# Kernel tuning notes

Measured on AMD Instinct MI355X. Metric: run time of the kernel, lower is better.

The kernel has to match this reference:

```python
import jax, jax.numpy as jnp
import numpy as np

DN = ('NCDHW', 'OIDHW', 'NCDHW')

def conv3d(x, w, b):
    # kernel (1,3,3), stride 1, padding (0,1,1)
    y = jax.lax.conv_general_dilated(x, w, window_strides=(1, 1, 1),
                                     padding=[(0, 0), (1, 1), (1, 1)],
                                     dimension_numbers=DN)
    return y + b[None, :, None, None, None]

def setup_inputs() -> dict:
    key = jax.random.key(0)
    ks = jax.random.split(key, 9)
    B, C, S, H, W = 16, 64, 64, 32, 32
    Cd = C // 2
    fan = C * 9
    sc = 1.0 / np.sqrt(fan)
    x = jax.random.normal(ks[0], (B, C, S, H, W), jnp.float32)
    wq = jax.random.normal(ks[1], (Cd, C, 1, 3, 3), jnp.float32) * sc
    bq = jax.random.normal(ks[2], (Cd,), jnp.float32) * sc
    wk = jax.random.normal(ks[3], (Cd, C, 1, 3, 3), jnp.float32) * sc
    bk = jax.random.normal(ks[4], (Cd,), jnp.float32) * sc
    wv = jax.random.normal(ks[5], (Cd, C, 1, 3, 3), jnp.float32) * sc
    bv = jax.random.normal(ks[6], (Cd,), jnp.float32) * sc
    wo = jax.random.normal(ks[7], (C, Cd, 1, 3, 3), jnp.float32) * (1.0 / np.sqrt(Cd * 9))
    bo = jax.random.normal(ks[8], (C,), jnp.float32) * (1.0 / np.sqrt(Cd * 9))
    return {"x": x, "wq": wq, "bq": bq, "wk": wk, "bk": bk,
            "wv": wv, "bv": bv, "wo": wo, "bo": bo}

def reference(x, wq, bq, wk, bk, wv, bv, wo, bo):
    B, C, S, H, W = x.shape
    scale = (H * W) ** (-0.5)
    q = conv3d(x, wq, bq).reshape(B, -1, S, H * W)  # (B, Cd, S, HW)
    k = conv3d(x, wk, bk).reshape(B, -1, S, H * W)
    v = conv3d(x, wv, bv).reshape(B, -1, S, H * W)
    # per-channel attention over sequence dim with sigmoid gate
    attn = jax.nn.sigmoid(jnp.einsum('bcsf,bctf->bcst', q, k) * scale)  # (B, Cd, S, S)
    out = jnp.einsum('bcst,bctf->bcsf', attn, v)  # (B, Cd, S, HW)
    out = out.reshape(B, -1, S, H, W)
    return conv3d(out, wo, bo)
```

## Files before the change

kernel.cpp:

```cpp
#include <hip/hip_runtime.h>
#include <hip/hip_bf16.h>

#define BB   16
#define CC   64
#define SS   64
#define HWHW 1024
#define CD   32
#define QELEMS (BB * CD * SS * HWHW)

typedef unsigned short ushort_t;
typedef __attribute__((ext_vector_type(8)))  short bf16x8;
typedef __attribute__((ext_vector_type(16))) float f32x16;

static __device__ inline float bf2f(ushort_t u) {
    union { float f; unsigned int i; } v;
    v.i = ((unsigned int)u) << 16;
    return v.f;
}
static __device__ inline ushort_t f2bf(float f) {
    union { float f; unsigned int i; } v;
    v.f = f;
    unsigned int x = v.i;
    return (ushort_t)((x + 0x7fffu + ((x >> 16) & 1u)) >> 16);
}

__global__ __launch_bounds__(256) void pack_weights(
    const float* __restrict__ wq, const float* __restrict__ wk,
    const float* __restrict__ wv, const float* __restrict__ wo,
    ushort_t* __restrict__ wt, ushort_t* __restrict__ wt2)
{
    const int d = blockIdx.x * 256 + threadIdx.x;
    if (d < 9 * 96 * 64) {
        const int tap = d / (96 * 64);
        const int rem = d % (96 * 64);
        const int oc  = rem >> 6;
        const int c   = rem & 63;
        const float* wsrc = (oc < 32) ? wq : (oc < 64) ? wk : wv;
        const int ocl = oc & 31;
        wt[d] = f2bf(wsrc[((size_t)ocl * 64 + c) * 9 + tap]);
    }
    const int d2 = d - 9 * 96 * 64;
    if (d2 >= 0 && d2 < 9 * 64 * 32) {
        const int tap = d2 / (64 * 32);
        const int rem = d2 % (64 * 32);
        const int oc  = rem >> 5;
        const int c   = rem & 31;
        wt2[d2] = f2bf(wo[((size_t)oc * 32 + c) * 9 + tap]);
    }
}

__global__ __launch_bounds__(256) void conv_qkv_mfma(
    const float* __restrict__ x,
    const ushort_t* __restrict__ wt,
    const float* __restrict__ bq, const float* __restrict__ bk,
    const float* __restrict__ bv,
    ushort_t* __restrict__ qkv)
{
    __shared__ ushort_t xs[10][34][72];

    const int tid   = threadIdx.x;
    const int bs    = blockIdx.x >> 2;
    const int chunk = blockIdx.x & 3;
    const int b     = bs >> 6;
    const int s     = bs & 63;
    const int h0    = chunk * 8;

    if (tid < 160) {
        const int r    = tid >> 4;
        const int rest = tid & 15;
        const int col  = (rest >> 3) ? 33 : 0;
        const int c0   = (rest & 7) << 3;
        bf16x8 z = {0, 0, 0, 0, 0, 0, 0, 0};
        *(bf16x8*)&xs[r][col][c0] = z;
    }

    const float* xb = x + ((size_t)b * CC * SS + s) * HWHW;
#pragma unroll
    for (int it = 0; it < 20; ++it) {
        const int u  = tid + it * 256;
        const int g  = u & 7;
        const int t2 = u >> 3;
        const int r  = t2 % 10;
        const int c  = t2 / 10;
        const int h  = h0 - 1 + r;
        float4 xv = make_float4(0.f, 0.f, 0.f, 0.f);
        if (h >= 0 && h < 32)
            xv = *(const float4*)(xb + (size_t)c * SS * HWHW + h * 32 + g * 4);
        const int colb = 1 + g * 4;
        xs[r][colb + 0][c] = f2bf(xv.x);
        xs[r][colb + 1][c] = f2bf(xv.y);
        xs[r][colb + 2][c] = f2bf(xv.z);
        xs[r][colb + 3][c] = f2bf(xv.w);
    }
    __syncthreads();

    const int wvid = tid >> 6;
    const int lane = tid & 63;
    const int ln   = lane & 31;
    const int lh   = lane >> 5;
    const int nt0  = wvid * 2;

    f32x16 acc[3][2];
#pragma unroll
    for (int m = 0; m < 3; ++m)
#pragma unroll
        for (int n = 0; n < 2; ++n)
#pragma unroll
            for (int i = 0; i < 16; ++i) acc[m][n][i] = 0.f;

#pragma unroll 1
    for (int tap = 0; tap < 9; ++tap) {
        const int dh = tap / 3;
        const int dw = tap % 3;
        const ushort_t* wtap = wt + (size_t)tap * 96 * 64;
#pragma unroll
        for (int kc = 0; kc < 4; ++kc) {
            const int c0 = kc * 16 + lh * 8;
            const bf16x8 a0 = *(const bf16x8*)(wtap + (((size_t)ln      ) << 6) + c0);
            const bf16x8 a1 = *(const bf16x8*)(wtap + (((size_t)ln + 32 ) << 6) + c0);
            const bf16x8 a2 = *(const bf16x8*)(wtap + (((size_t)ln + 64 ) << 6) + c0);
            const bf16x8 b0 = *(const bf16x8*)&xs[nt0 + dh    ][ln + dw][c0];
            const bf16x8 b1 = *(const bf16x8*)&xs[nt0 + 1 + dh][ln + dw][c0];
            acc[0][0] = __builtin_amdgcn_mfma_f32_32x32x16_bf16(a0, b0, acc[0][0], 0, 0, 0);
            acc[0][1] = __builtin_amdgcn_mfma_f32_32x32x16_bf16(a0, b1, acc[0][1], 0, 0, 0);
            acc[1][0] = __builtin_amdgcn_mfma_f32_32x32x16_bf16(a1, b0, acc[1][0], 0, 0, 0);
            acc[1][1] = __builtin_amdgcn_mfma_f32_32x32x16_bf16(a1, b1, acc[1][1], 0, 0, 0);
            acc[2][0] = __builtin_amdgcn_mfma_f32_32x32x16_bf16(a2, b0, acc[2][0], 0, 0, 0);
            acc[2][1] = __builtin_amdgcn_mfma_f32_32x32x16_bf16(a2, b1, acc[2][1], 0, 0, 0);
        }
    }

    const float* biases[3] = {bq, bk, bv};
#pragma unroll
    for (int mt = 0; mt < 3; ++mt) {
        const float* bptr = biases[mt];
        ushort_t* dst = qkv + (size_t)mt * QELEMS + (((size_t)b * CD) * SS + s) * HWHW;
#pragma unroll
        for (int ntl = 0; ntl < 2; ++ntl) {
            const int gp = (h0 + nt0 + ntl) * 32 + ln;
#pragma unroll
            for (int r = 0; r < 16; ++r) {
                const int m = (r & 3) + 8 * (r >> 2) + 4 * lh;
                const float val = acc[mt][ntl][r] + bptr[m];
                dst[(size_t)m * SS * HWHW + gp] = f2bf(val);
            }
        }
    }
}

__global__ __launch_bounds__(256) void attn_kernel(ushort_t* __restrict__ qkv)
{
    __shared__ float    scb[64][65];
    __shared__ ushort_t qch[64][132];
    __shared__ ushort_t kch[64][132];

    const int tid = threadIdx.x;
    const int bc  = blockIdx.x;
    ushort_t* qbase = qkv + (size_t)bc * SS * HWHW;
    const ushort_t* kbase = qbase + QELEMS;
    const ushort_t* vbase = qbase + 2 * (size_t)QELEMS;

    const int ty = tid >> 4, tx = tid & 15;
    const int sy = ty * 4, sx = tx * 4;

    float acc[4][4];
#pragma unroll
    for (int i = 0; i < 4; ++i)
#pragma unroll
        for (int j = 0; j < 4; ++j) acc[i][j] = 0.0f;

    for (int fc = 0; fc < 8; ++fc) {
        __syncthreads();
#pragma unroll
        for (int u = 0; u < 8; ++u) {
            const int unit = tid + u * 256;
            const int row  = unit >> 5;
            const int col  = (unit & 31) * 4;
            const ushort4 qa = *(const ushort4*)(qbase + (size_t)row * HWHW + fc * 128 + col);
            const ushort4 ka = *(const ushort4*)(kbase + (size_t)row * HWHW + fc * 128 + col);
            *(ushort4*)&qch[row][col] = qa;
            *(ushort4*)&kch[row][col] = ka;
        }
        __syncthreads();

        for (int f = 0; f < 128; f += 2) {
            float q0[4], q1[4], k0[4], k1[4];
#pragma unroll
            for (int i = 0; i < 4; ++i) {
                const unsigned int qp = *(const unsigned int*)&qch[sy + i][f];
                q0[i] = bf2f((ushort_t)(qp & 0xffffu));
                q1[i] = bf2f((ushort_t)(qp >> 16));
                const unsigned int kp = *(const unsigned int*)&kch[sx + i][f];
                k0[i] = bf2f((ushort_t)(kp & 0xffffu));
                k1[i] = bf2f((ushort_t)(kp >> 16));
            }
#pragma unroll
            for (int i = 0; i < 4; ++i)
#pragma unroll
                for (int j = 0; j < 4; ++j)
                    acc[i][j] += q0[i] * k0[j] + q1[i] * k1[j];
        }
    }

    const float scale = 0.03125f;
#pragma unroll
    for (int i = 0; i < 4; ++i)
#pragma unroll
        for (int j = 0; j < 4; ++j) {
            const float xv = acc[i][j] * scale;
            scb[sy + i][sx + j] = 1.0f / (1.0f + __expf(-xv));
        }
    __syncthreads();

    const int fcol = tid * 4;
#pragma unroll 1
    for (int gIdx = 0; gIdx < 4; ++gIdx) {
        float o[16][4];
#pragma unroll
        for (int i = 0; i < 16; ++i)
#pragma unroll
            for (int j = 0; j < 4; ++j) o[i][j] = 0.0f;

        for (int t = 0; t < 64; ++t) {
            const ushort4 va = *(const ushort4*)(vbase + (size_t)t * HWHW + fcol);
            const float v0 = bf2f(va.x), v1 = bf2f(va.y), v2 = bf2f(va.z), v3 = bf2f(va.w);
#pragma unroll
            for (int i = 0; i < 16; ++i) {
                const float a = scb[gIdx * 16 + i][t];
                o[i][0] += a * v0;
                o[i][1] += a * v1;
                o[i][2] += a * v2;
                o[i][3] += a * v3;
            }
        }
#pragma unroll
        for (int i = 0; i < 16; ++i) {
            const int srow = gIdx * 16 + i;
            ushort4 u;
            u.x = f2bf(o[i][0]);
            u.y = f2bf(o[i][1]);
            u.z = f2bf(o[i][2]);
            u.w = f2bf(o[i][3]);
            *(ushort4*)(qbase + (size_t)srow * HWHW + fcol) = u;
        }
    }
}

__global__ __launch_bounds__(256) void conv_out_mfma(
    const ushort_t* __restrict__ att,
    const ushort_t* __restrict__ wt2,
    const float* __restrict__ bo,
    float* __restrict__ out)
{
    __shared__ ushort_t xs[10][34][40];

    const int tid   = threadIdx.x;
    const int bs    = blockIdx.x >> 2;
    const int chunk = blockIdx.x & 3;
    const int b     = bs >> 6;
    const int s     = bs & 63;
    const int h0    = chunk * 8;

    if (tid < 80) {
        const int r    = tid >> 3;
        const int rest = tid & 7;
        const int col  = (rest >> 2) ? 33 : 0;
        const int c0   = (rest & 3) << 3;
        bf16x8 z = {0, 0, 0, 0, 0, 0, 0, 0};
        *(bf16x8*)&xs[r][col][c0] = z;
    }

    const ushort_t* ab = att + ((size_t)b * CD * SS + s) * HWHW;
#pragma unroll
    for (int it = 0; it < 10; ++it) {
        const int u  = tid + it * 256;
        const int g  = u & 7;
        const int t2 = u >> 3;
        const int r  = t2 % 10;
        const int c  = t2 / 10;
        const int h  = h0 - 1 + r;
        ushort4 xv = make_ushort4(0, 0, 0, 0);
        if (h >= 0 && h < 32)
            xv = *(const ushort4*)(ab + (size_t)c * SS * HWHW + h * 32 + g * 4);
        const int colb = 1 + g * 4;
        xs[r][colb + 0][c] = xv.x;
        xs[r][colb + 1][c] = xv.y;
        xs[r][colb + 2][c] = xv.z;
        xs[r][colb + 3][c] = xv.w;
    }
    __syncthreads();

    const int wvid = tid >> 6;
    const int lane = tid & 63;
    const int ln   = lane & 31;
    const int lh   = lane >> 5;
    const int nt0  = wvid * 2;

    f32x16 acc[2][2];
#pragma unroll
    for (int m = 0; m < 2; ++m)
#pragma unroll
        for (int n = 0; n < 2; ++n)
#pragma unroll
            for (int i = 0; i < 16; ++i) acc[m][n][i] = 0.f;

#pragma unroll 1
    for (int tap = 0; tap < 9; ++tap) {
        const int dh = tap / 3;
        const int dw = tap % 3;
        const ushort_t* wtap = wt2 + (size_t)tap * 64 * 32;
#pragma unroll
        for (int kc = 0; kc < 2; ++kc) {
            const int c0 = kc * 16 + lh * 8;
            const bf16x8 a0 = *(const bf16x8*)(wtap + (((size_t)ln      ) << 5) + c0);
            const bf16x8 a1 = *(const bf16x8*)(wtap + (((size_t)ln + 32 ) << 5) + c0);
            const bf16x8 b0 = *(const bf16x8*)&xs[nt0 + dh    ][ln + dw][c0];
            const bf16x8 b1 = *(const bf16x8*)&xs[nt0 + 1 + dh][ln + dw][c0];
            acc[0][0] = __builtin_amdgcn_mfma_f32_32x32x16_bf16(a0, b0, acc[0][0], 0, 0, 0);
            acc[0][1] = __builtin_amdgcn_mfma_f32_32x32x16_bf16(a0, b1, acc[0][1], 0, 0, 0);
            acc[1][0] = __builtin_amdgcn_mfma_f32_32x32x16_bf16(a1, b0, acc[1][0], 0, 0, 0);
            acc[1][1] = __builtin_amdgcn_mfma_f32_32x32x16_bf16(a1, b1, acc[1][1], 0, 0, 0);
        }
    }

#pragma unroll
    for (int mt = 0; mt < 2; ++mt) {
        float* dst = out + (((size_t)b * CC + mt * 32) * SS + s) * HWHW;
#pragma unroll
        for (int ntl = 0; ntl < 2; ++ntl) {
            const int gp = (h0 + nt0 + ntl) * 32 + ln;
#pragma unroll
            for (int r = 0; r < 16; ++r) {
                const int m = (r & 3) + 8 * (r >> 2) + 4 * lh;
                dst[(size_t)m * SS * HWHW + gp] = acc[mt][ntl][r] + bo[mt * 32 + m];
            }
        }
    }
}

extern "C" void kernel_launch(void* const* d_in, const int* in_sizes, int n_in,
                              void* d_out, int out_size, void* d_ws, size_t ws_size,
                              hipStream_t stream)
{
    const float* x  = (const float*)d_in[0];
    const float* wq = (const float*)d_in[1];
    const float* bq = (const float*)d_in[2];
    const float* wk = (const float*)d_in[3];
    const float* bk = (const float*)d_in[4];
    const float* wv = (const float*)d_in[5];
    const float* bv = (const float*)d_in[6];
    const float* wo = (const float*)d_in[7];
    const float* bo = (const float*)d_in[8];
    float* out = (float*)d_out;

    ushort_t* qkv = (ushort_t*)d_ws;
    ushort_t* wt  = (ushort_t*)((char*)d_ws + (size_t)3 * QELEMS * 2);
    ushort_t* wt2 = wt + 9 * 96 * 64;

    pack_weights<<<288, 256, 0, stream>>>(wq, wk, wv, wo, wt, wt2);
    conv_qkv_mfma<<<dim3(BB * SS * 4), 256, 0, stream>>>(x, wt, bq, bk, bv, qkv);
    attn_kernel<<<dim3(BB * CD), 256, 0, stream>>>(qkv);
    conv_out_mfma<<<dim3(BB * SS * 4), 256, 0, stream>>>(qkv, wt2, bo, out);
}
```

Measured before the change: 1.083 ms.

## Pre-transpose conv inputs to channel-last bf16 for vectorized tile loads

Adds two transpose kernels that convert x (fp32 NCDHW) and the attention output into per-(b,s) pixel-major, channel-contiguous bf16 buffers. Both conv kernels then fill their LDS tiles with 16-byte vector loads and stores instead of scalar strided LDS writes with a per-element conversion. The xT buffer reuses the output buffer as scratch and attT reuses the K slot of the qkv workspace. The cost is two extra launches and an extra full read and write pass over the input and attention tensors.

```diff
diff --git a/kernel.cpp b/kernel.cpp
--- a/kernel.cpp
+++ b/kernel.cpp
@@ -49,8 +49,82 @@
     }
 }
 
+__global__ __launch_bounds__(256) void transpose_x(
+    const float* __restrict__ x, ushort_t* __restrict__ xT)
+{
+    __shared__ ushort_t t[64][132];
+
+    const int bs  = blockIdx.x;
+    const int b   = bs >> 6;
+    const int s   = bs & 63;
+    const int tid = threadIdx.x;
+    const float* xb = x + ((size_t)b * CC * SS + s) * HWHW;
+    ushort_t*    xo = xT + (size_t)bs * HWHW * CC;
+
+    for (int fc = 0; fc < 8; ++fc) {
+        __syncthreads();
+#pragma unroll
+        for (int i = 0; i < 8; ++i) {
+            const int u  = tid + i * 256;
+            const int c  = u >> 5;
+            const int f4 = u & 31;
+            const float4 v = *(const float4*)(xb + (size_t)c * SS * HWHW + fc * 128 + f4 * 4);
+            const unsigned int lo = (unsigned int)f2bf(v.x) | ((unsigned int)f2bf(v.y) << 16);
+            const unsigned int hi = (unsigned int)f2bf(v.z) | ((unsigned int)f2bf(v.w) << 16);
+            *(uint2*)&t[c][f4 * 4] = make_uint2(lo, hi);
+        }
+        __syncthreads();
+#pragma unroll
+        for (int i = 0; i < 4; ++i) {
+            const int u  = tid + i * 256;
+            const int px = u >> 3;
+            const int cg = (u & 7) * 8;
+            bf16x8 vv;
+#pragma unroll
+            for (int j = 0; j < 8; ++j) vv[j] = (short)t[cg + j][px];
+            *(bf16x8*)(xo + (size_t)(fc * 128 + px) * CC + cg) = vv;
+        }
+    }
+}
+
+__global__ __launch_bounds__(256) void transpose_att(
+    const ushort_t* __restrict__ att, ushort_t* __restrict__ attT)
+{
+    __shared__ ushort_t t[32][260];
+
+    const int bs  = blockIdx.x;
+    const int b   = bs >> 6;
+    const int s   = bs & 63;
+    const int tid = threadIdx.x;
+    const ushort_t* ab = att + ((size_t)b * CD * SS + s) * HWHW;
+    ushort_t*       ao = attT + (size_t)bs * HWHW * CD;
+
+    for (int fc = 0; fc < 4; ++fc) {
+        __syncthreads();
+#pragma unroll
+        for (int i = 0; i < 8; ++i) {
+            const int u  = tid + i * 256;
+            const int c  = u >> 6;
+            const int f4 = u & 63;
+            const ushort4 v = *(const ushort4*)(ab + (size_t)c * SS * HWHW + fc * 256 + f4 * 4);
+            *(ushort4*)&t[c][f4 * 4] = v;
+        }
+        __syncthreads();
+#pragma unroll
+        for (int i = 0; i < 4; ++i) {
+            const int u  = tid + i * 256;
+            const int px = u >> 2;
+            const int cg = (u & 3) * 8;
+            bf16x8 vv;
+#pragma unroll
+            for (int j = 0; j < 8; ++j) vv[j] = (short)t[cg + j][px];
+            *(bf16x8*)(ao + (size_t)(fc * 256 + px) * CD + cg) = vv;
+        }
+    }
+}
+
 __global__ __launch_bounds__(256) void conv_qkv_mfma(
-    const float* __restrict__ x,
+    const ushort_t* __restrict__ xT,
     const ushort_t* __restrict__ wt,
     const float* __restrict__ bq, const float* __restrict__ bk,
     const float* __restrict__ bv,
@@ -74,23 +148,18 @@
         *(bf16x8*)&xs[r][col][c0] = z;
     }
 
-    const float* xb = x + ((size_t)b * CC * SS + s) * HWHW;
-#pragma unroll
-    for (int it = 0; it < 20; ++it) {
-        const int u  = tid + it * 256;
-        const int g  = u & 7;
-        const int t2 = u >> 3;
-        const int r  = t2 % 10;
-        const int c  = t2 / 10;
-        const int h  = h0 - 1 + r;
-        float4 xv = make_float4(0.f, 0.f, 0.f, 0.f);
-        if (h >= 0 && h < 32)
-            xv = *(const float4*)(xb + (size_t)c * SS * HWHW + h * 32 + g * 4);
-        const int colb = 1 + g * 4;
-        xs[r][colb + 0][c] = f2bf(xv.x);
-        xs[r][colb + 1][c] = f2bf(xv.y);
-        xs[r][colb + 2][c] = f2bf(xv.z);
-        xs[r][colb + 3][c] = f2bf(xv.w);
+    const ushort_t* xb = xT + (size_t)bs * HWHW * CC;
+    {
+        const int w  = tid >> 3;
+        const int cg = (tid & 7) * 8;
+#pragma unroll
+        for (int it = 0; it < 10; ++it) {
+            const int h = h0 - 1 + it;
+            bf16x8 v = {0, 0, 0, 0, 0, 0, 0, 0};
+            if (h >= 0 && h < 32)
+                v = *(const bf16x8*)(xb + (size_t)(h * 32 + w) * CC + cg);
+            *(bf16x8*)&xs[it][1 + w][cg] = v;
+        }
     }
     __syncthreads();
 
@@ -247,7 +316,7 @@
 }
 
 __global__ __launch_bounds__(256) void conv_out_mfma(
-    const ushort_t* __restrict__ att,
+    const ushort_t* __restrict__ attT,
     const ushort_t* __restrict__ wt2,
     const float* __restrict__ bo,
     float* __restrict__ out)
@@ -270,23 +339,18 @@
         *(bf16x8*)&xs[r][col][c0] = z;
     }
 
-    const ushort_t* ab = att + ((size_t)b * CD * SS + s) * HWHW;
-#pragma unroll
-    for (int it = 0; it < 10; ++it) {
+    const ushort_t* ab = attT + (size_t)bs * HWHW * CD;
+#pragma unroll
+    for (int it = 0; it < 5; ++it) {
         const int u  = tid + it * 256;
-        const int g  = u & 7;
-        const int t2 = u >> 3;
-        const int r  = t2 % 10;
-        const int c  = t2 / 10;
+        const int cg = (u & 3) * 8;
+        const int w  = (u >> 2) & 31;
+        const int r  = u >> 7;
         const int h  = h0 - 1 + r;
-        ushort4 xv = make_ushort4(0, 0, 0, 0);
+        bf16x8 v = {0, 0, 0, 0, 0, 0, 0, 0};
         if (h >= 0 && h < 32)
-            xv = *(const ushort4*)(ab + (size_t)c * SS * HWHW + h * 32 + g * 4);
-        const int colb = 1 + g * 4;
-        xs[r][colb + 0][c] = xv.x;
-        xs[r][colb + 1][c] = xv.y;
-        xs[r][colb + 2][c] = xv.z;
-        xs[r][colb + 3][c] = xv.w;
+            v = *(const bf16x8*)(ab + (size_t)(h * 32 + w) * CD + cg);
+        *(bf16x8*)&xs[r][1 + w][cg] = v;
     }
     __syncthreads();
 
@@ -356,9 +420,13 @@
     ushort_t* qkv = (ushort_t*)d_ws;
     ushort_t* wt  = (ushort_t*)((char*)d_ws + (size_t)3 * QELEMS * 2);
     ushort_t* wt2 = wt + 9 * 96 * 64;
-
+    ushort_t* xT   = (ushort_t*)d_out;
+    ushort_t* attT = qkv + (size_t)QELEMS;
+
+    transpose_x<<<dim3(BB * SS), 256, 0, stream>>>(x, xT);
     pack_weights<<<288, 256, 0, stream>>>(wq, wk, wv, wo, wt, wt2);
-    conv_qkv_mfma<<<dim3(BB * SS * 4), 256, 0, stream>>>(x, wt, bq, bk, bv, qkv);
+    conv_qkv_mfma<<<dim3(BB * SS * 4), 256, 0, stream>>>(xT, wt, bq, bk, bv, qkv);
     attn_kernel<<<dim3(BB * CD), 256, 0, stream>>>(qkv);
-    conv_out_mfma<<<dim3(BB * SS * 4), 256, 0, stream>>>(qkv, wt2, bo, out);
-}
+    transpose_att<<<dim3(BB * SS), 256, 0, stream>>>(qkv, attT);
+    conv_out_mfma<<<dim3(BB * SS * 4), 256, 0, stream>>>(attT, wt2, bo, out);
+}
```

Result: faster. 1.028 ms (-5.1%).
